# Optimization experiments

Hardware: AMD Instinct MI355X
Metric: run time of the kernel (lower is better)

The kernel has to match this reference:

```python
import jax, jax.numpy as jnp
import numpy as np

NUM_EXPERTS = 8
TOP_K = 2
B, S, H, I = 4, 4096, 1024, 2048


def setup_inputs() -> dict:
    key = jax.random.key(0)
    ks = jax.random.split(key, 4)
    std = 0.02
    return {
        "hidden_states": jax.random.normal(ks[0], (B, S, H), dtype=jnp.float32),
        "w_gate": jax.random.normal(ks[1], (NUM_EXPERTS, H), dtype=jnp.float32) * std,
        "w_fc": jax.random.normal(ks[2], (NUM_EXPERTS, I, H), dtype=jnp.float32) * std,
        "b_fc": jnp.zeros((NUM_EXPERTS, I), dtype=jnp.float32),
        "w_proj": jax.random.normal(ks[3], (NUM_EXPERTS, H, I), dtype=jnp.float32) * (std / np.sqrt(2 * 24)),
        "b_proj": jnp.zeros((NUM_EXPERTS, H), dtype=jnp.float32),
    }


def reference(hidden_states, w_gate, w_fc, b_fc, w_proj, b_proj):
    b, s, h = hidden_states.shape
    x = hidden_states.reshape(-1, h)  # [T, H]
    # routing: top-k over gate logits, softmax over the k selected logits
    router_logits = jnp.einsum("th,eh->te", x, w_gate)  # [T, E]
    top_vals, top_idx = jax.lax.top_k(router_logits, TOP_K)  # [T, K]
    gates = jax.nn.softmax(top_vals.astype(jnp.float32), axis=-1).astype(x.dtype)  # [T, K]
    # expert MLPs with weighted combine; per-token gate for expert e is the
    # selected routing weight (0 if e not in top-k) -- same math as the
    # gather / grouped-GEMM / index_add scatter in the original.
    out = jnp.zeros_like(x)
    for e in range(NUM_EXPERTS):
        g_e = jnp.sum(jnp.where(top_idx == e, gates, jnp.zeros_like(gates)), axis=-1)  # [T]
        hmid = jax.nn.gelu(x @ w_fc[e].T + b_fc[e], approximate=False)  # [T, I]
        y = hmid @ w_proj[e].T + b_proj[e]  # [T, H]
        out = out + g_e[:, None] * y
    return out.reshape(b, s, h)
```

## Files before the change

### kernel.cpp

```cpp
#include <hip/hip_runtime.h>
#include <math.h>

#define T_TOK 16384
#define HDIM  1024
#define IDIM  2048
#define NEXP  8
#define CAP   16384

typedef __bf16 bf16x8 __attribute__((ext_vector_type(8)));
typedef float  f32x4  __attribute__((ext_vector_type(4)));
typedef unsigned short us8 __attribute__((ext_vector_type(8)));

__device__ __forceinline__ unsigned short f2bf(float f) {
  unsigned int u = __builtin_bit_cast(unsigned int, f);
  u = (u + 0x7FFFu + ((u >> 16) & 1u)) >> 16;
  return (unsigned short)u;
}

__device__ __forceinline__ float bf2f(unsigned short u) {
  return __builtin_bit_cast(float, (unsigned int)u << 16);
}

__device__ __forceinline__ void gld16(const void* g, void* l) {
  __builtin_amdgcn_global_load_lds(
      (const __attribute__((address_space(1))) void*)(g),
      (__attribute__((address_space(3))) void*)(l), 16, 0, 0);
}

__device__ __forceinline__ bf16x8 cvt8(const float* p) {
  f32x4 lo = *(const f32x4*)p;
  f32x4 hi = *(const f32x4*)(p + 4);
  us8 t;
  t[0] = f2bf(lo[0]); t[1] = f2bf(lo[1]); t[2] = f2bf(lo[2]); t[3] = f2bf(lo[3]);
  t[4] = f2bf(hi[0]); t[5] = f2bf(hi[1]); t[6] = f2bf(hi[2]); t[7] = f2bf(hi[3]);
  return __builtin_bit_cast(bf16x8, t);
}

__global__ void zero_out_k(float4* out) {
  out[blockIdx.x * 256 + threadIdx.x] = float4{0.f, 0.f, 0.f, 0.f};
}

__global__ void report_k(float* out, float v, int n) {
  int idx = blockIdx.x * blockDim.x + threadIdx.x;
  int stride = gridDim.x * blockDim.x;
  for (int i = idx; i < n; i += stride) out[i] = v;
}

__global__ void cvt_bf16_k(const float* __restrict__ src, unsigned short* __restrict__ dst, int n4) {
  int idx = blockIdx.x * blockDim.x + threadIdx.x;
  int stride = gridDim.x * blockDim.x;
  for (int i = idx; i < n4; i += stride) {
    float4 v = ((const float4*)src)[i];
    ushort4 o;
    o.x = f2bf(v.x); o.y = f2bf(v.y); o.z = f2bf(v.z); o.w = f2bf(v.w);
    ((ushort4*)dst)[i] = o;
  }
}

__global__ void route1_k(const float* __restrict__ x, const float* __restrict__ wg,
                         int* __restrict__ echoice, float* __restrict__ tgate) {
  __shared__ __align__(16) float wgl[NEXP * HDIM];
  int tid = threadIdx.x;
  for (int i = tid; i < NEXP * HDIM / 4; i += 256)
    ((float4*)wgl)[i] = ((const float4*)wg)[i];
  __syncthreads();

  int wave = tid >> 6, lane = tid & 63;
  int t = blockIdx.x * 4 + wave;

  float accv[NEXP];
#pragma unroll
  for (int e = 0; e < NEXP; e++) accv[e] = 0.f;
  const float* xr = x + (size_t)t * HDIM;
#pragma unroll 4
  for (int j = 0; j < HDIM / 64; j++) {
    float xv = xr[lane + j * 64];
#pragma unroll
    for (int e = 0; e < NEXP; e++) accv[e] += xv * wgl[e * HDIM + lane + j * 64];
  }
#pragma unroll
  for (int off = 1; off < 64; off <<= 1) {
#pragma unroll
    for (int e = 0; e < NEXP; e++) accv[e] += __shfl_xor(accv[e], off, 64);
  }

  if (lane == 0) {
    int e0 = 0; float v0 = accv[0];
#pragma unroll
    for (int e = 1; e < NEXP; e++) if (accv[e] > v0) { v0 = accv[e]; e0 = e; }
    int e1 = -1; float v1 = -3.4e38f;
#pragma unroll
    for (int e = 0; e < NEXP; e++) if (e != e0 && accv[e] > v1) { v1 = accv[e]; e1 = e; }
    float ex = expf(v1 - v0);
    echoice[t] = e0 | (e1 << 8);
    tgate[t * 2]     = 1.f / (1.f + ex);
    tgate[t * 2 + 1] = ex / (1.f + ex);
  }
}

__global__ void route2_k(const int* __restrict__ echoice, int* __restrict__ counts,
                         int* __restrict__ etok) {
  int E = blockIdx.x;
  int tid = threadIdx.x, lane = tid & 63, wv = tid >> 6;
  __shared__ int base;
  __shared__ int wsum[4];
  if (tid == 0) base = 0;
  __syncthreads();
  for (int t0 = 0; t0 < T_TOK; t0 += 256) {
    int t = t0 + tid;
    int ec = echoice[t];
    int e0 = ec & 255, e1 = (ec >> 8) & 255;
    bool m = (e0 == E) | (e1 == E);
    int code = t * 2 + (e1 == E ? 1 : 0);
    unsigned long long mask = __ballot(m);
    if (lane == 0) wsum[wv] = __popcll(mask);
    int lpre = __popcll(mask & ((1ull << lane) - 1ull));
    __syncthreads();
    int wbase = 0;
#pragma unroll
    for (int w = 0; w < 4; w++) if (w < wv) wbase += wsum[w];
    int total = wsum[0] + wsum[1] + wsum[2] + wsum[3];
    if (m) etok[E * CAP + base + wbase + lpre] = code;
    __syncthreads();
    if (tid == 0) base += total;
    __syncthreads();
  }
  if (tid == 0) counts[E] = base;
}

template <int STAGE, int K, int N, bool A32, bool B32, bool YATOM>
__global__ __launch_bounds__(256)
void gemm_k(const void* __restrict__ Ap_, const void* __restrict__ Wp_,
            const float* __restrict__ bias, unsigned short* __restrict__ hmid,
            unsigned short* __restrict__ ybf, float* __restrict__ out,
            const float* __restrict__ tgate,
            const int* __restrict__ counts, const int* __restrict__ etok) {
  constexpr int NT = N / 128;
  constexpr int ASZ = A32 ? 16384 : 8192;
  constexpr int BSZ = B32 ? 16384 : 8192;
  __shared__ __align__(16) char smem[ASZ + BSZ];
  char* As = smem;
  char* Bs = smem + ASZ;

  int e  = blockIdx.x / (128 * NT);
  int bi = blockIdx.x % (128 * NT);
  int rt = bi / NT, ct = bi % NT;
  int cnt = counts[e];
  if (rt * 128 >= cnt) return;

  int tid = threadIdx.x;
  int lane = tid & 63, wv = tid >> 6;
  int wr = wv >> 1, wc = wv & 1;
  int quad = lane >> 4, ml = lane & 15;

  const char* aptr[4];
  if constexpr (A32) {
    int srow = tid >> 3, seg = tid & 7;
    const float* Af = (const float*)Ap_;
#pragma unroll
    for (int q = 0; q < 4; q++) {
      int r = rt * 128 + q * 32 + srow;
      int code = etok[e * CAP + (r < cnt ? r : cnt - 1)];
      int row = (STAGE == 1) ? (code >> 1) : code;
      aptr[q] = (const char*)(Af + (size_t)row * K + seg * 4);
    }
  } else {
    int srow = tid >> 2, seg = tid & 3;
    const unsigned short* Ab = (const unsigned short*)Ap_;
#pragma unroll
    for (int q = 0; q < 2; q++) {
      int r = rt * 128 + q * 64 + srow;
      int code = etok[e * CAP + (r < cnt ? r : cnt - 1)];
      int row = (STAGE == 1) ? (code >> 1) : code;
      aptr[q] = (const char*)(Ab + (size_t)row * K + seg * 8);
    }
  }
  const char* bptr[4];
  if constexpr (B32) {
    int srow = tid >> 3, seg = tid & 7;
    const float* Wf = (const float*)Wp_;
#pragma unroll
    for (int q = 0; q < 4; q++)
      bptr[q] = (const char*)(Wf + ((size_t)e * N + ct * 128 + q * 32 + srow) * K + seg * 4);
  } else {
    int srow = tid >> 2, seg = tid & 3;
    const unsigned short* Wb = (const unsigned short*)Wp_;
#pragma unroll
    for (int q = 0; q < 2; q++)
      bptr[q] = (const char*)(Wb + ((size_t)e * N + ct * 128 + q * 64 + srow) * K + seg * 8);
  }

  f32x4 acc[4][4] = {};

  for (int k0 = 0; k0 < K; k0 += 32) {
    size_t aoff = (size_t)k0 * (A32 ? 4 : 2);
    size_t boff = (size_t)k0 * (B32 ? 4 : 2);
    if constexpr (A32) {
#pragma unroll
      for (int q = 0; q < 4; q++) gld16(aptr[q] + aoff, As + q * 4096 + tid * 16);
    } else {
#pragma unroll
      for (int q = 0; q < 2; q++) gld16(aptr[q] + aoff, As + q * 4096 + tid * 16);
    }
    if constexpr (B32) {
#pragma unroll
      for (int q = 0; q < 4; q++) gld16(bptr[q] + boff, Bs + q * 4096 + tid * 16);
    } else {
#pragma unroll
      for (int q = 0; q < 2; q++) gld16(bptr[q] + boff, Bs + q * 4096 + tid * 16);
    }
    __syncthreads();

    bf16x8 af[4], bfr[4];
#pragma unroll
    for (int mi = 0; mi < 4; mi++) {
      int row = wr * 64 + mi * 16 + ml;
      if constexpr (A32) af[mi] = cvt8((const float*)As + row * 32 + quad * 8);
      else af[mi] = __builtin_bit_cast(bf16x8, *(const us8*)((const unsigned short*)As + row * 32 + quad * 8));
    }
#pragma unroll
    for (int ni = 0; ni < 4; ni++) {
      int row = wc * 64 + ni * 16 + ml;
      if constexpr (B32) bfr[ni] = cvt8((const float*)Bs + row * 32 + quad * 8);
      else bfr[ni] = __builtin_bit_cast(bf16x8, *(const us8*)((const unsigned short*)Bs + row * 32 + quad * 8));
    }
#pragma unroll
    for (int mi = 0; mi < 4; mi++)
#pragma unroll
      for (int ni = 0; ni < 4; ni++)
        acc[mi][ni] = __builtin_amdgcn_mfma_f32_16x16x32_bf16(af[mi], bfr[ni], acc[mi][ni], 0, 0, 0);
    __syncthreads();
  }

#pragma unroll
  for (int mi = 0; mi < 4; mi++) {
    int ms[4], codes[4];
#pragma unroll
    for (int r = 0; r < 4; r++) {
      ms[r] = rt * 128 + wr * 64 + mi * 16 + quad * 4 + r;
      codes[r] = etok[e * CAP + (ms[r] < cnt ? ms[r] : 0)];
    }
#pragma unroll
    for (int ni = 0; ni < 4; ni++) {
      int n = ct * 128 + wc * 64 + ni * 16 + ml;
      float bv = bias[e * N + n];
#pragma unroll
      for (int r = 0; r < 4; r++) {
        if (ms[r] < cnt) {
          float v = acc[mi][ni][r] + bv;
          if (STAGE == 1) {
            v = 0.5f * v * (1.0f + erff(v * 0.70710678118654752f));
            hmid[(size_t)codes[r] * IDIM + n] = f2bf(v);
          } else if (YATOM) {
            atomicAdd(&out[(size_t)(codes[r] >> 1) * HDIM + n], tgate[codes[r]] * v);
          } else {
            ybf[(size_t)codes[r] * HDIM + n] = f2bf(v);
          }
        }
      }
    }
  }
}

__global__ void combine_k(const unsigned short* __restrict__ y, const float* __restrict__ tgate,
                          float* __restrict__ out) {
  int idx = blockIdx.x * 256 + threadIdx.x;
  int t = idx >> 7;
  int c = idx & 127;
  float g0 = tgate[t * 2], g1 = tgate[t * 2 + 1];
  us8 a = *(const us8*)(y + ((size_t)(t * 2) * HDIM) + c * 8);
  us8 b = *(const us8*)(y + ((size_t)(t * 2 + 1) * HDIM) + c * 8);
  float o[8];
#pragma unroll
  for (int i = 0; i < 8; i++) o[i] = g0 * bf2f(a[i]) + g1 * bf2f(b[i]);
  float4* op = (float4*)(out + (size_t)t * HDIM + c * 8);
  op[0] = float4{o[0], o[1], o[2], o[3]};
  op[1] = float4{o[4], o[5], o[6], o[7]};
}

extern "C" void kernel_launch(void* const* d_in, const int* in_sizes, int n_in,
                              void* d_out, int out_size, void* d_ws, size_t ws_size,
                              hipStream_t stream) {
  const float* x     = (const float*)d_in[0];
  const float* wg    = (const float*)d_in[1];
  const float* wfc   = (const float*)d_in[2];
  const float* bfc   = (const float*)d_in[3];
  const float* wproj = (const float*)d_in[4];
  const float* bproj = (const float*)d_in[5];
  float* out = (float*)d_out;

  char* ws = (char*)d_ws;
  size_t off = 0;
  int* counts  = (int*)(ws + off);   off += 4096;
  int* echoice = (int*)(ws + off);   off += (size_t)T_TOK * 4;
  int* etok    = (int*)(ws + off);   off += (size_t)NEXP * CAP * 4;
  float* tgate = (float*)(ws + off); off += (size_t)T_TOK * 2 * 4;
  unsigned short* hmid = (unsigned short*)(ws + off);
  off += (size_t)T_TOK * 2 * IDIM * 2;
  size_t lean_need = off;
  unsigned short* xbf = (unsigned short*)(ws + off);
  size_t off2 = off + (size_t)T_TOK * HDIM * 2;
  unsigned short* wfcbf = (unsigned short*)(ws + off2);
  off2 += (size_t)NEXP * IDIM * HDIM * 2;
  unsigned short* wprojbf = (unsigned short*)(ws + off2);
  off2 += (size_t)NEXP * HDIM * IDIM * 2;
  size_t full_need = off2;
  unsigned short* ybf = xbf;

  if (ws_size < lean_need) {
    report_k<<<256, 256, 0, stream>>>(out, (float)(ws_size >> 20), T_TOK * HDIM);
    return;
  }

  route1_k<<<T_TOK / 4, 256, 0, stream>>>(x, wg, echoice, tgate);
  route2_k<<<NEXP, 256, 0, stream>>>(echoice, counts, etok);

  if (ws_size >= full_need) {
    cvt_bf16_k<<<4096, 256, 0, stream>>>(x,     xbf,     T_TOK * HDIM / 4);
    cvt_bf16_k<<<4096, 256, 0, stream>>>(wfc,   wfcbf,   NEXP * IDIM * HDIM / 4);
    cvt_bf16_k<<<4096, 256, 0, stream>>>(wproj, wprojbf, NEXP * HDIM * IDIM / 4);
    gemm_k<1, HDIM, IDIM, false, false, false><<<NEXP * 128 * (IDIM / 128), 256, 0, stream>>>(
        xbf, wfcbf, bfc, hmid, ybf, out, tgate, counts, etok);
    gemm_k<2, IDIM, HDIM, false, false, false><<<NEXP * 128 * (HDIM / 128), 256, 0, stream>>>(
        hmid, wprojbf, bproj, hmid, ybf, out, tgate, counts, etok);
    combine_k<<<T_TOK * HDIM / 8 / 256, 256, 0, stream>>>(ybf, tgate, out);
  } else {
    zero_out_k<<<T_TOK * HDIM / 1024, 256, 0, stream>>>((float4*)out);
    gemm_k<1, HDIM, IDIM, true, true, true><<<NEXP * 128 * (IDIM / 128), 256, 0, stream>>>(
        x, wfc, bfc, hmid, ybf, out, tgate, counts, etok);
    gemm_k<2, IDIM, HDIM, false, true, true><<<NEXP * 128 * (HDIM / 128), 256, 0, stream>>>(
        hmid, wproj, bproj, hmid, ybf, out, tgate, counts, etok);
  }
}
```

Before: 737.2 us.

## Add 256x256-tile 8-wave grouped GEMM with 4-stage async LDS pipeline

Replaces both expert GEMM launches on the bf16 path with a new kernel. It uses 256x256 output tiles, 512 threads (8 waves), and a 4-deep global_load_lds ring buffer in 128KB of dynamic shared memory. Loads are interleaved with split MFMA phases, separated by barriers and setprio. The larger tiles are meant to raise data reuse and hide global-load latency. In exchange, occupancy drops to one block per CU and padding waste grows when an expert's token count is not a multiple of 256.

```diff
diff --git a/kernel.cpp b/kernel.cpp
--- a/kernel.cpp
+++ b/kernel.cpp
@@ -6,6 +6,7 @@
 #define IDIM  2048
 #define NEXP  8
 #define CAP   16384
+#define ROWT  (CAP / 256)
 
 typedef __bf16 bf16x8 __attribute__((ext_vector_type(8)));
 typedef float  f32x4  __attribute__((ext_vector_type(4)));
@@ -128,6 +129,136 @@
   if (tid == 0) counts[E] = base;
 }
 
+template <int STAGE, int K, int N>
+__global__ __launch_bounds__(512)
+void gemm8_k(const unsigned short* __restrict__ A, const unsigned short* __restrict__ W,
+             const float* __restrict__ bias, unsigned short* __restrict__ hmid,
+             unsigned short* __restrict__ ybf,
+             const int* __restrict__ counts, const int* __restrict__ etok) {
+  extern __shared__ __align__(16) char smem[];
+  constexpr int NTK = K / 32;
+  constexpr int NTC = N / 256;
+  int e  = blockIdx.x / (ROWT * NTC);
+  int bi = blockIdx.x % (ROWT * NTC);
+  int rt = bi / NTC, ct = bi % NTC;
+  int cnt = counts[e];
+  if (rt * 256 >= cnt) return;
+
+  int tid = threadIdx.x;
+  int lane = tid & 63, wv = tid >> 6;
+  int wr = wv >> 2, wc = wv & 3;
+  int quad = lane >> 4, ml = lane & 15;
+
+  int sg = tid >> 6, sq = (tid >> 4) & 3, sml = tid & 15;
+  const unsigned short* aptr[2];
+  const unsigned short* bptr[2];
+#pragma unroll
+  for (int h = 0; h < 2; h++) {
+    int r = rt * 256 + h * 128 + sg * 16 + sml;
+    int code = etok[e * CAP + (r < cnt ? r : cnt - 1)];
+    int arow = (STAGE == 1) ? (code >> 1) : code;
+    aptr[h] = A + (size_t)arow * K + sq * 8;
+    int n = ct * 256 + h * 128 + sg * 16 + sml;
+    bptr[h] = W + ((size_t)e * N + n) * K + sq * 8;
+  }
+  char* Asm = smem;
+  char* Bsm = smem + 65536;
+  int ldst = tid * 16;
+
+  auto stage_a = [&](int t) {
+    int tt = t < NTK ? t : NTK - 1;
+    char* dst = Asm + ((t & 3) * 2) * 8192 + ldst;
+    gld16(aptr[0] + (size_t)tt * 32, dst);
+    gld16(aptr[1] + (size_t)tt * 32, dst + 8192);
+  };
+  auto stage_b = [&](int t) {
+    int tt = t < NTK ? t : NTK - 1;
+    char* dst = Bsm + ((t & 3) * 2) * 8192 + ldst;
+    gld16(bptr[0] + (size_t)tt * 32, dst);
+    gld16(bptr[1] + (size_t)tt * 32, dst + 8192);
+  };
+
+  f32x4 acc[8][4] = {};
+
+  stage_a(0); stage_b(0);
+  stage_a(1); stage_b(1);
+  stage_a(2); stage_b(2);
+  asm volatile("s_waitcnt vmcnt(8)" ::: "memory");
+  __builtin_amdgcn_s_barrier();
+
+  int aoff = quad * 256 + ml * 16;
+  int boff = (wc & 1) * 4096 + quad * 256 + ml * 16;
+
+#pragma unroll 4
+  for (int t = 0; t < NTK; t++) {
+    const char* Ah = Asm + ((t & 3) * 2 + wr) * 8192;
+    const char* Bh = Bsm + ((t & 3) * 2 + (wc >> 1)) * 8192;
+    bf16x8 b0[4], a0[4];
+#pragma unroll
+    for (int ni = 0; ni < 4; ni++) b0[ni] = *(const bf16x8*)(Bh + boff + ni * 1024);
+#pragma unroll
+    for (int mi = 0; mi < 4; mi++) a0[mi] = *(const bf16x8*)(Ah + aoff + mi * 1024);
+    stage_a(t + 3);
+    asm volatile("" ::: "memory");
+    __builtin_amdgcn_s_barrier();
+    __builtin_amdgcn_s_setprio(1);
+#pragma unroll
+    for (int mi = 0; mi < 4; mi++)
+#pragma unroll
+      for (int ni = 0; ni < 4; ni++)
+        acc[mi][ni] = __builtin_amdgcn_mfma_f32_16x16x32_bf16(a0[mi], b0[ni], acc[mi][ni], 0, 0, 0);
+    __builtin_amdgcn_s_setprio(0);
+    asm volatile("" ::: "memory");
+    __builtin_amdgcn_s_barrier();
+    bf16x8 a1[4];
+#pragma unroll
+    for (int mi = 0; mi < 4; mi++) a1[mi] = *(const bf16x8*)(Ah + aoff + (4 + mi) * 1024);
+    stage_b(t + 3);
+    asm volatile("" ::: "memory");
+    __builtin_amdgcn_s_barrier();
+    __builtin_amdgcn_s_setprio(1);
+#pragma unroll
+    for (int mi = 0; mi < 4; mi++)
+#pragma unroll
+      for (int ni = 0; ni < 4; ni++)
+        acc[4 + mi][ni] = __builtin_amdgcn_mfma_f32_16x16x32_bf16(a1[mi], b0[ni], acc[4 + mi][ni], 0, 0, 0);
+    __builtin_amdgcn_s_setprio(0);
+    asm volatile("s_waitcnt vmcnt(8)" ::: "memory");
+    __builtin_amdgcn_s_barrier();
+  }
+
+  int ncol[4]; float bv[4];
+#pragma unroll
+  for (int ni = 0; ni < 4; ni++) {
+    ncol[ni] = ct * 256 + wc * 64 + ni * 16 + ml;
+    bv[ni] = bias[e * N + ncol[ni]];
+  }
+#pragma unroll
+  for (int mi = 0; mi < 8; mi++) {
+    int ms[4], codes[4];
+#pragma unroll
+    for (int r = 0; r < 4; r++) {
+      ms[r] = rt * 256 + wr * 128 + mi * 16 + quad * 4 + r;
+      codes[r] = etok[e * CAP + (ms[r] < cnt ? ms[r] : 0)];
+    }
+#pragma unroll
+    for (int ni = 0; ni < 4; ni++) {
+#pragma unroll
+      for (int r = 0; r < 4; r++) {
+        if (ms[r] < cnt) {
+          float v = acc[mi][ni][r] + bv[ni];
+          if (STAGE == 1) {
+            v = 0.5f * v * (1.0f + erff(v * 0.70710678118654752f));
+            hmid[(size_t)codes[r] * IDIM + ncol[ni]] = f2bf(v);
+          } else {
+            ybf[(size_t)codes[r] * HDIM + ncol[ni]] = f2bf(v);
+          }
+        }
+      }
+    }
+  }
+}
+
 template <int STAGE, int K, int N, bool A32, bool B32, bool YATOM>
 __global__ __launch_bounds__(256)
 void gemm_k(const void* __restrict__ Ap_, const void* __restrict__ Wp_,
@@ -138,9 +269,9 @@
   constexpr int NT = N / 128;
   constexpr int ASZ = A32 ? 16384 : 8192;
   constexpr int BSZ = B32 ? 16384 : 8192;
-  __shared__ __align__(16) char smem[ASZ + BSZ];
-  char* As = smem;
-  char* Bs = smem + ASZ;
+  __shared__ __align__(16) char smem_s[ASZ + BSZ];
+  char* As = smem_s;
+  char* Bs = smem_s + ASZ;
 
   int e  = blockIdx.x / (128 * NT);
   int bi = blockIdx.x % (128 * NT);
@@ -243,11 +374,11 @@
 #pragma unroll
     for (int ni = 0; ni < 4; ni++) {
       int n = ct * 128 + wc * 64 + ni * 16 + ml;
-      float bv = bias[e * N + n];
+      float bvv = bias[e * N + n];
 #pragma unroll
       for (int r = 0; r < 4; r++) {
         if (ms[r] < cnt) {
-          float v = acc[mi][ni][r] + bv;
+          float v = acc[mi][ni][r] + bvv;
           if (STAGE == 1) {
             v = 0.5f * v * (1.0f + erff(v * 0.70710678118654752f));
             hmid[(size_t)codes[r] * IDIM + n] = f2bf(v);
@@ -316,13 +447,21 @@
   route2_k<<<NEXP, 256, 0, stream>>>(echoice, counts, etok);
 
   if (ws_size >= full_need) {
+    static bool s_attr = false;
+    if (!s_attr) {
+      (void)hipFuncSetAttribute((const void*)gemm8_k<1, HDIM, IDIM>,
+                                hipFuncAttributeMaxDynamicSharedMemorySize, 131072);
+      (void)hipFuncSetAttribute((const void*)gemm8_k<2, IDIM, HDIM>,
+                                hipFuncAttributeMaxDynamicSharedMemorySize, 131072);
+      s_attr = true;
+    }
     cvt_bf16_k<<<4096, 256, 0, stream>>>(x,     xbf,     T_TOK * HDIM / 4);
     cvt_bf16_k<<<4096, 256, 0, stream>>>(wfc,   wfcbf,   NEXP * IDIM * HDIM / 4);
     cvt_bf16_k<<<4096, 256, 0, stream>>>(wproj, wprojbf, NEXP * HDIM * IDIM / 4);
-    gemm_k<1, HDIM, IDIM, false, false, false><<<NEXP * 128 * (IDIM / 128), 256, 0, stream>>>(
-        xbf, wfcbf, bfc, hmid, ybf, out, tgate, counts, etok);
-    gemm_k<2, IDIM, HDIM, false, false, false><<<NEXP * 128 * (HDIM / 128), 256, 0, stream>>>(
-        hmid, wprojbf, bproj, hmid, ybf, out, tgate, counts, etok);
+    gemm8_k<1, HDIM, IDIM><<<NEXP * ROWT * (IDIM / 256), 512, 131072, stream>>>(
+        xbf, wfcbf, bfc, hmid, ybf, counts, etok);
+    gemm8_k<2, IDIM, HDIM><<<NEXP * ROWT * (HDIM / 256), 512, 131072, stream>>>(
+        hmid, wprojbf, bproj, hmid, ybf, counts, etok);
     combine_k<<<T_TOK * HDIM / 8 / 256, 256, 0, stream>>>(ybf, tgate, out);
   } else {
     zero_out_k<<<T_TOK * HDIM / 1024, 256, 0, stream>>>((float4*)out);
```

Result: slower. 817.2 us (+10.8%).

## Fuse x bf16 conversion into routing and use fragment-ordered LDS layout

Applied to the files above, without the earlier changes.

The routing kernel now writes the bf16 copy of x while it reads x for the gate logits, so the separate conversion pass over the activations is dropped. The bf16 GEMM path also changes how rows are mapped to LDS slots: each 16-row by 32-k block is stored in MFMA fragment order, so every lane reads one contiguous 16-byte chunk at lane*16. This is meant to remove LDS bank conflicts and cut address arithmetic in the inner loop. The trade-off is that the routing kernel's bf16 stores are 2-byte scalar writes, and the global loads now have a different coalescing pattern.

```diff
diff --git a/kernel.cpp b/kernel.cpp
--- a/kernel.cpp
+++ b/kernel.cpp
@@ -58,7 +58,8 @@
 }
 
 __global__ void route1_k(const float* __restrict__ x, const float* __restrict__ wg,
-                         int* __restrict__ echoice, float* __restrict__ tgate) {
+                         int* __restrict__ echoice, float* __restrict__ tgate,
+                         unsigned short* __restrict__ xbf) {
   __shared__ __align__(16) float wgl[NEXP * HDIM];
   int tid = threadIdx.x;
   for (int i = tid; i < NEXP * HDIM / 4; i += 256)
@@ -75,6 +76,7 @@
 #pragma unroll 4
   for (int j = 0; j < HDIM / 64; j++) {
     float xv = xr[lane + j * 64];
+    if (xbf) xbf[(size_t)t * HDIM + lane + j * 64] = f2bf(xv);
 #pragma unroll
     for (int e = 0; e < NEXP; e++) accv[e] += xv * wgl[e * HDIM + lane + j * 64];
   }
@@ -153,6 +155,8 @@
   int wr = wv >> 1, wc = wv & 1;
   int quad = lane >> 4, ml = lane & 15;
 
+  int fml = tid & 15, fq = (tid >> 4) & 3, fg = tid >> 6;
+
   const char* aptr[4];
   if constexpr (A32) {
     int srow = tid >> 3, seg = tid & 7;
@@ -165,14 +169,13 @@
       aptr[q] = (const char*)(Af + (size_t)row * K + seg * 4);
     }
   } else {
-    int srow = tid >> 2, seg = tid & 3;
     const unsigned short* Ab = (const unsigned short*)Ap_;
 #pragma unroll
     for (int q = 0; q < 2; q++) {
-      int r = rt * 128 + q * 64 + srow;
+      int r = rt * 128 + (q * 4 + fg) * 16 + fml;
       int code = etok[e * CAP + (r < cnt ? r : cnt - 1)];
       int row = (STAGE == 1) ? (code >> 1) : code;
-      aptr[q] = (const char*)(Ab + (size_t)row * K + seg * 8);
+      aptr[q] = (const char*)(Ab + (size_t)row * K + fq * 8);
     }
   }
   const char* bptr[4];
@@ -183,11 +186,10 @@
     for (int q = 0; q < 4; q++)
       bptr[q] = (const char*)(Wf + ((size_t)e * N + ct * 128 + q * 32 + srow) * K + seg * 4);
   } else {
-    int srow = tid >> 2, seg = tid & 3;
     const unsigned short* Wb = (const unsigned short*)Wp_;
 #pragma unroll
     for (int q = 0; q < 2; q++)
-      bptr[q] = (const char*)(Wb + ((size_t)e * N + ct * 128 + q * 64 + srow) * K + seg * 8);
+      bptr[q] = (const char*)(Wb + ((size_t)e * N + ct * 128 + (q * 4 + fg) * 16 + fml) * K + fq * 8);
   }
 
   f32x4 acc[4][4] = {};
@@ -214,15 +216,21 @@
     bf16x8 af[4], bfr[4];
 #pragma unroll
     for (int mi = 0; mi < 4; mi++) {
-      int row = wr * 64 + mi * 16 + ml;
-      if constexpr (A32) af[mi] = cvt8((const float*)As + row * 32 + quad * 8);
-      else af[mi] = __builtin_bit_cast(bf16x8, *(const us8*)((const unsigned short*)As + row * 32 + quad * 8));
+      if constexpr (A32) {
+        int row = wr * 64 + mi * 16 + ml;
+        af[mi] = cvt8((const float*)As + row * 32 + quad * 8);
+      } else {
+        af[mi] = __builtin_bit_cast(bf16x8, *(const us8*)(As + (wr * 4 + mi) * 1024 + lane * 16));
+      }
     }
 #pragma unroll
     for (int ni = 0; ni < 4; ni++) {
-      int row = wc * 64 + ni * 16 + ml;
-      if constexpr (B32) bfr[ni] = cvt8((const float*)Bs + row * 32 + quad * 8);
-      else bfr[ni] = __builtin_bit_cast(bf16x8, *(const us8*)((const unsigned short*)Bs + row * 32 + quad * 8));
+      if constexpr (B32) {
+        int row = wc * 64 + ni * 16 + ml;
+        bfr[ni] = cvt8((const float*)Bs + row * 32 + quad * 8);
+      } else {
+        bfr[ni] = __builtin_bit_cast(bf16x8, *(const us8*)(Bs + (wc * 4 + ni) * 1024 + lane * 16));
+      }
     }
 #pragma unroll
     for (int mi = 0; mi < 4; mi++)
@@ -312,11 +320,12 @@
     return;
   }
 
-  route1_k<<<T_TOK / 4, 256, 0, stream>>>(x, wg, echoice, tgate);
+  bool full = (ws_size >= full_need);
+
+  route1_k<<<T_TOK / 4, 256, 0, stream>>>(x, wg, echoice, tgate, full ? xbf : (unsigned short*)nullptr);
   route2_k<<<NEXP, 256, 0, stream>>>(echoice, counts, etok);
 
-  if (ws_size >= full_need) {
-    cvt_bf16_k<<<4096, 256, 0, stream>>>(x,     xbf,     T_TOK * HDIM / 4);
+  if (full) {
     cvt_bf16_k<<<4096, 256, 0, stream>>>(wfc,   wfcbf,   NEXP * IDIM * HDIM / 4);
     cvt_bf16_k<<<4096, 256, 0, stream>>>(wproj, wprojbf, NEXP * HDIM * IDIM / 4);
     gemm_k<1, HDIM, IDIM, false, false, false><<<NEXP * 128 * (IDIM / 128), 256, 0, stream>>>(
```

Measured after the change: 934.5 us. 26.8% more time.
